# Kernel tuning notes

Measured on AMD Instinct MI355X. Metric: run time of the kernel, lower is better.

Reference implementation:

```python
import jax, jax.numpy as jnp
import numpy as np

N = 100          # num_objects
H = 128          # decoder_hidden
D = 128          # input_size (== H, required by the module's GRU linears)
REL = 7          # num_relative_features (use_3d=False)
E = N * (N - 1)  # fully-connected, no self loops
B = 32

_mask = ~np.eye(N, dtype=bool)
_SEND_NP, _RECV_NP = np.where(_mask)  # torch.where(~eye): rows=send, cols=recv
SEND = jnp.asarray(_SEND_NP, dtype=jnp.int32)
RECV = jnp.asarray(_RECV_NP, dtype=jnp.int32)


def setup_inputs() -> dict:
    key = jax.random.key(0)
    ks = jax.random.split(key, 34)
    def w(k, shape, scale=0.05):
        return jax.random.normal(k, shape, dtype=jnp.float32) * scale
    inp = {
        "inputs": jax.random.normal(ks[0], (B, N, D), jnp.float32),
        "edge_attr": jax.random.normal(ks[1], (B, E, REL + D), jnp.float32),
        "hidden": jax.random.normal(ks[2], (B, N, H), jnp.float32),
        # msg_mlp: Linear(2H,H) Tanh Linear(H,H) Tanh
        "msg_w1": w(ks[3], (2 * H, H)), "msg_b1": w(ks[4], (H,)),
        "msg_w2": w(ks[5], (H, H)),     "msg_b2": w(ks[6], (H,)),
        # present_msg_mlp: Linear(REL+D,H) ReLU Linear(H,H) ReLU
        "pm_w1": w(ks[7], (REL + D, H)), "pm_b1": w(ks[8], (H,)),
        "pm_w2": w(ks[9], (H, H)),       "pm_b2": w(ks[10], (H,)),
        # res_mlp: Linear(D,H) ReLU Linear(H,H) ReLU
        "res_w1": w(ks[11], (D, H)), "res_b1": w(ks[12], (H,)),
        "res_w2": w(ks[13], (H, H)), "res_b2": w(ks[14], (H,)),
        # GRU-style gates
        "ir_w": w(ks[15], (H, H)), "ir_b": w(ks[16], (H,)),
        "ii_w": w(ks[17], (H, H)), "ii_b": w(ks[18], (H,)),
        "in_w": w(ks[19], (H, H)), "in_b": w(ks[20], (H,)),
        "hr_w": w(ks[21], (H, H)),
        "hi_w": w(ks[22], (H, H)),
        "hh_w": w(ks[23], (H, H)),
        # out_mlp: Linear(H,H) ReLU Linear(H,H) ReLU Linear(H,D)
        "out_w1": w(ks[24], (H, H)), "out_b1": w(ks[25], (H,)),
        "out_w2": w(ks[26], (H, H)), "out_b2": w(ks[27], (H,)),
        "out_w3": w(ks[28], (H, D)), "out_b3": w(ks[29], (D,)),
    }
    return inp


def _scatter_mean(msgs, recv, num_nodes):
    # msgs: [B, E, H] -> [B, N, H], mean over incoming edges per node
    counts = jnp.zeros((num_nodes,), msgs.dtype).at[recv].add(1.0)
    summed = jnp.zeros((msgs.shape[0], num_nodes, msgs.shape[-1]), msgs.dtype)
    summed = summed.at[:, recv].add(msgs)
    return summed / counts[None, :, None]


def reference(inputs, edge_attr, hidden,
              msg_w1, msg_b1, msg_w2, msg_b2,
              pm_w1, pm_b1, pm_w2, pm_b2,
              res_w1, res_b1, res_w2, res_b2,
              ir_w, ir_b, ii_w, ii_b, in_w, in_b,
              hr_w, hi_w, hh_w,
              out_w1, out_b1, out_w2, out_b2, out_w3, out_b3):
    # gather hidden states along edges (dropout is identity: p=0 / eval)
    hm = jnp.concatenate([hidden[:, RECV], hidden[:, SEND]], axis=-1)  # [B,E,2H]
    hm = jnp.tanh(jnp.tanh(hm @ msg_w1 + msg_b1) @ msg_w2 + msg_b2)
    hidden_node = _scatter_mean(hm, RECV, N)                           # [B,N,H]

    pm = jax.nn.relu(jax.nn.relu(edge_attr @ pm_w1 + pm_b1) @ pm_w2 + pm_b2)
    present_node = _scatter_mean(pm, RECV, N)
    present_node = present_node + jax.nn.relu(
        jax.nn.relu(inputs @ res_w1 + res_b1) @ res_w2 + res_b2)

    r = jax.nn.sigmoid(present_node @ ir_w + ir_b + hidden_node @ hr_w)
    i = jax.nn.sigmoid(present_node @ ii_w + ii_b + hidden_node @ hi_w)
    n = jnp.tanh(present_node @ in_w + in_b + r * (hidden_node @ hh_w))
    hidden_new = (1.0 - i) * n + i * hidden

    pred = jax.nn.relu(hidden_new @ out_w1 + out_b1)
    pred = jax.nn.relu(pred @ out_w2 + out_b2)
    pred = pred @ out_w3 + out_b3
    return pred, hidden_new
```

## Files before the change

### kernel.cpp

```cpp
#include <hip/hip_runtime.h>

typedef unsigned short u16;
typedef unsigned int   u32;
typedef __attribute__((ext_vector_type(8))) short bf8;
typedef __attribute__((ext_vector_type(4))) float f4;

#define DF __device__ __forceinline__

DF float bf2f(u16 h){ u32 u = ((u32)h) << 16; float f; __builtin_memcpy(&f, &u, 4); return f; }
DF u16 f2bf(float f){ u32 u; __builtin_memcpy(&u, &f, 4); u = (u + 0x7FFFu + ((u >> 16) & 1u)) >> 16; return (u16)u; }
DF float fexp2(float x){ return __builtin_amdgcn_exp2f(x); }
DF float frcp (float x){ return __builtin_amdgcn_rcpf(x); }
DF float tanhF(float x){ float e = fexp2(2.8853900817779268f * x); return 1.0f - 2.0f * frcp(e + 1.0f); }
DF float sigF (float x){ return frcp(1.0f + fexp2(-1.4426950408889634f * x)); }
DF float4 ld4u(const float* p){ float4 v; __builtin_memcpy(&v, p, 16); return v; }
DF u32 cvtpk(float lo, float hi){ u32 r; asm("v_cvt_pk_bf16_f32 %0, %1, %2" : "=v"(r) : "v"(lo), "v"(hi)); return r; }

DF const bf8* fragp(const u16* packed, int w, int nt, int ks, int lane){
  return reinterpret_cast<const bf8*>(packed + (((w * 32 + nt * 4 + ks) * 64 + lane) * 8));
}
DF const bf8* fragp_pm1(const u16* packed, int nt, int ks, int lane){
  return reinterpret_cast<const bf8*>(packed + (((512 + nt * 5 + ks) * 64 + lane) * 8));
}

struct WPtrs { const float* p[16]; };

__global__ __launch_bounds__(256) void k_pack(WPtrs wp, u16* __restrict__ packed){
  int bi = blockIdx.x;
  int lane = threadIdx.x & 63, warp = threadIdx.x >> 6;
  if(bi == 16){
    const float* __restrict__ src = wp.p[14];
    u16* __restrict__ dst = packed + 512 * 64 * 8;
    for(int i = warp; i < 40; i += 4){
      int nt = i / 5, ks = i - nt * 5;
      int col = nt * 16 + (lane & 15);
      int kb  = ks * 32 + (lane >> 4) * 8;
      u16* o = dst + (i * 64 + lane) * 8;
      for(int j = 0; j < 8; j++){
        int row = kb + j;
        o[j] = (row < 135) ? f2bf(src[row * 128 + col]) : (u16)0;
      }
    }
    return;
  }
  const float* __restrict__ src = wp.p[bi];
  u16* __restrict__ dst = packed + bi * 32 * 64 * 8;
  for(int i = warp; i < 32; i += 4){
    int nt = i >> 2, ks = i & 3;
    int col = nt * 16 + (lane & 15);
    int kb  = ks * 32 + (lane >> 4) * 8;
    u16* o = dst + (i * 64 + lane) * 8;
    for(int j = 0; j < 8; j++) o[j] = f2bf(src[(kb + j) * 128 + col]);
  }
}

__global__ __launch_bounds__(512) void k_node_pre(
    const float* __restrict__ hidden, const float* __restrict__ inputs,
    const u16* __restrict__ packed,
    const float* __restrict__ res_b1, const float* __restrict__ res_b2,
    float* __restrict__ Ptop, float* __restrict__ Pbot, float* __restrict__ res2)
{
  __shared__ __align__(16) u16 hid[64 * 136];
  __shared__ __align__(16) u16 inp[64 * 136];
  __shared__ __align__(16) u16 t1s[64 * 136];
  int row0 = blockIdx.x * 64;
  int t = threadIdx.x, lane = t & 63, w = t >> 6;
  int lrow = lane & 15, lk = lane >> 4;
  for(int i = t; i < 64 * 128; i += 512){
    int rr = i >> 7, cc = i & 127;
    hid[rr * 136 + cc] = f2bf(hidden[(row0 + rr) * 128 + cc]);
    inp[rr * 136 + cc] = f2bf(inputs[(row0 + rr) * 128 + cc]);
  }
  bf8 f0[4], f1[4], f5[4], f6[4];
  #pragma unroll
  for(int k = 0; k < 4; k++){
    f0[k] = *fragp(packed, 0, w, k, lane);
    f1[k] = *fragp(packed, 1, w, k, lane);
    f5[k] = *fragp(packed, 5, w, k, lane);
    f6[k] = *fragp(packed, 6, w, k, lane);
  }
  int col = w * 16 + lrow;
  float rb1 = res_b1[col], rb2 = res_b2[col];
  __syncthreads();
  #pragma unroll
  for(int m = 0; m < 4; m++){
    bf8 a[4], a2[4];
    #pragma unroll
    for(int k = 0; k < 4; k++){
      a[k]  = *reinterpret_cast<const bf8*>(&hid[(m * 16 + lrow) * 136 + k * 32 + lk * 8]);
      a2[k] = *reinterpret_cast<const bf8*>(&inp[(m * 16 + lrow) * 136 + k * 32 + lk * 8]);
    }
    f4 c0 = {0.f,0.f,0.f,0.f}, c1 = {0.f,0.f,0.f,0.f}, c2 = {0.f,0.f,0.f,0.f};
    #pragma unroll
    for(int k = 0; k < 4; k++){
      c0 = __builtin_amdgcn_mfma_f32_16x16x32_bf16(a[k],  f0[k], c0, 0, 0, 0);
      c1 = __builtin_amdgcn_mfma_f32_16x16x32_bf16(a[k],  f1[k], c1, 0, 0, 0);
      c2 = __builtin_amdgcn_mfma_f32_16x16x32_bf16(a2[k], f5[k], c2, 0, 0, 0);
    }
    #pragma unroll
    for(int q = 0; q < 4; q++){
      int gr = row0 + m * 16 + lk * 4 + q;
      Ptop[gr * 128 + col] = c0[q];
      Pbot[gr * 128 + col] = c1[q];
      float v = c2[q] + rb1; v = v > 0.f ? v : 0.f;
      t1s[(m * 16 + lk * 4 + q) * 136 + col] = f2bf(v);
    }
  }
  __syncthreads();
  #pragma unroll
  for(int m = 0; m < 4; m++){
    bf8 a3[4];
    #pragma unroll
    for(int k = 0; k < 4; k++)
      a3[k] = *reinterpret_cast<const bf8*>(&t1s[(m * 16 + lrow) * 136 + k * 32 + lk * 8]);
    f4 c = {0.f,0.f,0.f,0.f};
    #pragma unroll
    for(int k = 0; k < 4; k++)
      c = __builtin_amdgcn_mfma_f32_16x16x32_bf16(a3[k], f6[k], c, 0, 0, 0);
    #pragma unroll
    for(int q = 0; q < 4; q++){
      float v = c[q] + rb2; v = v > 0.f ? v : 0.f;
      res2[(row0 + m * 16 + lk * 4 + q) * 128 + col] = v;
    }
  }
}

__global__ __launch_bounds__(256, 5) void k_edge(
    const float* __restrict__ EA,
    const float* __restrict__ Ptop, const float* __restrict__ Pbot,
    const float* __restrict__ msg_b1, const float* __restrict__ msg_b2,
    const float* __restrict__ pm_b1, const float* __restrict__ pm_b2,
    const u16* __restrict__ packed,
    float* __restrict__ hnode, float* __restrict__ pnode)
{
  __shared__ __align__(16) u16 bufA[112 * 128];
  __shared__ __align__(16) u16 tail[112 * 8];
  char* bb = (char*)bufA;
  char* tb = (char*)tail;
  int blk = blockIdx.x;
  int b = blk / 100, r = blk - b * 100;
  int t = threadIdx.x, lane = t & 63, w = t >> 6;
  int lrow = lane & 15, lk = lane >> 4;
  int n0 = 2 * w, n1 = 2 * w + 1;

  {
    bf8 w1a[5], w1b[5];
    #pragma unroll
    for(int k = 0; k < 5; k++){ w1a[k] = *fragp_pm1(packed, n0, k, lane); w1b[k] = *fragp_pm1(packed, n1, k, lane); }
    float b1a = pm_b1[n0 * 16 + lrow], b1b = pm_b1[n1 * 16 + lrow];
    for(int i = t; i < 99 * 16; i += 256){
      int row = i >> 4, g = i & 15;
      int s = row + (row >= r ? 1 : 0);
      int e = s * 99 + (r < s ? r : r - 1);
      const float* rp = EA + ((size_t)(b * 9900 + e)) * 135 + g * 8;
      float4 v0 = ld4u(rp), v1 = ld4u(rp + 4);
      u32 pk[4] = {cvtpk(v0.x, v0.y), cvtpk(v0.z, v0.w), cvtpk(v1.x, v1.y), cvtpk(v1.z, v1.w)};
      *reinterpret_cast<uint4*>(bb + row * 256 + ((g ^ (row & 7)) << 4)) = *reinterpret_cast<const uint4*>(pk);
    }
    for(int row = t; row < 99; row += 256){
      int s = row + (row >= r ? 1 : 0);
      int e = s * 99 + (r < s ? r : r - 1);
      const float* rp = EA + ((size_t)(b * 9900 + e)) * 135 + 128;
      float4 v0 = ld4u(rp);
      u32 pk[4] = {cvtpk(v0.x, v0.y), cvtpk(v0.z, v0.w), cvtpk(rp[4], rp[5]), cvtpk(rp[6], 0.f)};
      *reinterpret_cast<uint4*>(tb + row * 16) = *reinterpret_cast<const uint4*>(pk);
    }
    __syncthreads();
    #pragma unroll
    for(int m = 0; m < 7; m++){
      int arow = m * 16 + lrow;
      int sw = (arow & 7);
      bf8 a[5];
      #pragma unroll
      for(int k = 0; k < 4; k++)
        a[k] = *reinterpret_cast<const bf8*>(bb + arow * 256 + (((k * 4 + lk) ^ sw) << 4));
      bf8 a4 = {0,0,0,0,0,0,0,0};
      if(lk == 0) a4 = *reinterpret_cast<const bf8*>(tb + arow * 16);
      f4 c0 = {0.f,0.f,0.f,0.f}, c1 = {0.f,0.f,0.f,0.f};
      #pragma unroll
      for(int k = 0; k < 4; k++){
        c0 = __builtin_amdgcn_mfma_f32_16x16x32_bf16(a[k], w1a[k], c0, 0, 0, 0);
        c1 = __builtin_amdgcn_mfma_f32_16x16x32_bf16(a[k], w1b[k], c1, 0, 0, 0);
      }
      c0 = __builtin_amdgcn_mfma_f32_16x16x32_bf16(a4, w1a[4], c0, 0, 0, 0);
      c1 = __builtin_amdgcn_mfma_f32_16x16x32_bf16(a4, w1b[4], c1, 0, 0, 0);
      __syncthreads();
      #pragma unroll
      for(int qp = 0; qp < 2; qp++){
        float v0 = c0[2*qp]   + b1a; v0 = v0 > 0.f ? v0 : 0.f;
        float u0 = c0[2*qp+1] + b1a; u0 = u0 > 0.f ? u0 : 0.f;
        float v1 = c1[2*qp]   + b1b; v1 = v1 > 0.f ? v1 : 0.f;
        float u1 = c1[2*qp+1] + b1b; u1 = u1 > 0.f ? u1 : 0.f;
        u32 p0 = cvtpk(v0, u0), p1 = cvtpk(v1, u1);
        int row0_ = m * 16 + lk * 4 + 2 * qp;
        int sw0 = (row0_ & 7) << 4, sw1 = ((row0_ + 1) & 7) << 4;
        *reinterpret_cast<u16*>(bb + row0_ * 256       + (((n0 * 16 + lrow) * 2) ^ sw0)) = (u16)p0;
        *reinterpret_cast<u16*>(bb + (row0_ + 1) * 256 + (((n0 * 16 + lrow) * 2) ^ sw1)) = (u16)(p0 >> 16);
        *reinterpret_cast<u16*>(bb + row0_ * 256       + (((n1 * 16 + lrow) * 2) ^ sw0)) = (u16)p1;
        *reinterpret_cast<u16*>(bb + (row0_ + 1) * 256 + (((n1 * 16 + lrow) * 2) ^ sw1)) = (u16)(p1 >> 16);
      }
    }
    __syncthreads();
    bf8 w2a[4], w2b[4];
    #pragma unroll
    for(int k = 0; k < 4; k++){ w2a[k] = *fragp(packed, 15, n0, k, lane); w2b[k] = *fragp(packed, 15, n1, k, lane); }
    float b2a = pm_b2[n0 * 16 + lrow], b2b = pm_b2[n1 * 16 + lrow];
    float acc0 = 0.f, acc1 = 0.f;
    #pragma unroll
    for(int m = 0; m < 7; m++){
      int arow = m * 16 + lrow;
      int sw = (arow & 7);
      bf8 a[4];
      #pragma unroll
      for(int k = 0; k < 4; k++)
        a[k] = *reinterpret_cast<const bf8*>(bb + arow * 256 + (((k * 4 + lk) ^ sw) << 4));
      f4 c0 = {0.f,0.f,0.f,0.f}, c1 = {0.f,0.f,0.f,0.f};
      #pragma unroll
      for(int k = 0; k < 4; k++){
        c0 = __builtin_amdgcn_mfma_f32_16x16x32_bf16(a[k], w2a[k], c0, 0, 0, 0);
        c1 = __builtin_amdgcn_mfma_f32_16x16x32_bf16(a[k], w2b[k], c1, 0, 0, 0);
      }
      #pragma unroll
      for(int q = 0; q < 4; q++){
        int rr = m * 16 + lk * 4 + q;
        if(rr < 99){
          float v0 = c0[q] + b2a; acc0 += (v0 > 0.f ? v0 : 0.f);
          float v1 = c1[q] + b2b; acc1 += (v1 > 0.f ? v1 : 0.f);
        }
      }
    }
    acc0 += __shfl_xor(acc0, 16); acc0 += __shfl_xor(acc0, 32);
    acc1 += __shfl_xor(acc1, 16); acc1 += __shfl_xor(acc1, 32);
    if(lane < 16){
      float* dst = pnode + ((size_t)b * 100 + r) * 128;
      dst[n0 * 16 + lane] = acc0 * (1.0f / 99.0f);
      dst[n1 * 16 + lane] = acc1 * (1.0f / 99.0f);
    }
  }
  __syncthreads();

  {
    bf8 w2a[4], w2b[4];
    #pragma unroll
    for(int k = 0; k < 4; k++){ w2a[k] = *fragp(packed, 13, n0, k, lane); w2b[k] = *fragp(packed, 13, n1, k, lane); }
    float b2a = msg_b2[n0 * 16 + lrow], b2b = msg_b2[n1 * 16 + lrow];
    int c4 = t & 31;
    float4 pt = *reinterpret_cast<const float4*>(Ptop + ((size_t)b * 100 + r) * 128 + c4 * 4);
    float4 mb = *reinterpret_cast<const float4*>(msg_b1 + c4 * 4);
    pt.x += mb.x; pt.y += mb.y; pt.z += mb.z; pt.w += mb.w;
    for(int row = t >> 5; row < 99; row += 8){
      int s = row + (row >= r ? 1 : 0);
      float4 v = *reinterpret_cast<const float4*>(Pbot + ((size_t)b * 100 + s) * 128 + c4 * 4);
      u32 pk[2] = {cvtpk(tanhF(pt.x + v.x), tanhF(pt.y + v.y)),
                   cvtpk(tanhF(pt.z + v.z), tanhF(pt.w + v.w))};
      *reinterpret_cast<uint2*>(bb + row * 256 + ((8 * c4) ^ ((row & 7) << 4))) = *reinterpret_cast<const uint2*>(pk);
    }
    __syncthreads();
    float acc0 = 0.f, acc1 = 0.f;
    #pragma unroll
    for(int m = 0; m < 7; m++){
      int arow = m * 16 + lrow;
      int sw = (arow & 7);
      bf8 a[4];
      #pragma unroll
      for(int k = 0; k < 4; k++)
        a[k] = *reinterpret_cast<const bf8*>(bb + arow * 256 + (((k * 4 + lk) ^ sw) << 4));
      f4 c0 = {0.f,0.f,0.f,0.f}, c1 = {0.f,0.f,0.f,0.f};
      #pragma unroll
      for(int k = 0; k < 4; k++){
        c0 = __builtin_amdgcn_mfma_f32_16x16x32_bf16(a[k], w2a[k], c0, 0, 0, 0);
        c1 = __builtin_amdgcn_mfma_f32_16x16x32_bf16(a[k], w2b[k], c1, 0, 0, 0);
      }
      #pragma unroll
      for(int q = 0; q < 4; q++){
        int rr = m * 16 + lk * 4 + q;
        if(rr < 99){
          acc0 += tanhF(c0[q] + b2a);
          acc1 += tanhF(c1[q] + b2b);
        }
      }
    }
    acc0 += __shfl_xor(acc0, 16); acc0 += __shfl_xor(acc0, 32);
    acc1 += __shfl_xor(acc1, 16); acc1 += __shfl_xor(acc1, 32);
    if(lane < 16){
      float* dst = hnode + ((size_t)b * 100 + r) * 128;
      dst[n0 * 16 + lane] = acc0 * (1.0f / 99.0f);
      dst[n1 * 16 + lane] = acc1 * (1.0f / 99.0f);
    }
  }
}

__global__ __launch_bounds__(512) void k_final(
    const float* __restrict__ hnode, const float* __restrict__ pnode,
    const float* __restrict__ res2, const float* __restrict__ hidden,
    const u16* __restrict__ packed,
    const float* __restrict__ ir_b, const float* __restrict__ ii_b, const float* __restrict__ in_b,
    const float* __restrict__ ob1, const float* __restrict__ ob2, const float* __restrict__ ob3,
    float* __restrict__ out_pred, float* __restrict__ out_hid)
{
  __shared__ __align__(16) u16 hn[64 * 136];
  __shared__ __align__(16) u16 pr[64 * 136];
  __shared__ __align__(16) u16 hw[64 * 136];
  int row0 = blockIdx.x * 64;
  int t = threadIdx.x, lane = t & 63, w = t >> 6;
  int lrow = lane & 15, lk = lane >> 4;
  for(int i = t; i < 64 * 128; i += 512){
    int rr = i >> 7, cc = i & 127;
    hn[rr * 136 + cc] = f2bf(hnode[(row0 + rr) * 128 + cc]);
    pr[rr * 136 + cc] = f2bf(pnode[(row0 + rr) * 128 + cc] + res2[(row0 + rr) * 128 + cc]);
  }
  int col = w * 16 + lrow;
  bf8 mhr[4], mhi[4], mhh[4], mir[4], mii[4], min_[4];
  #pragma unroll
  for(int k = 0; k < 4; k++){
    mhr[k]  = *fragp(packed, 2, w, k, lane);
    mhi[k]  = *fragp(packed, 3, w, k, lane);
    mhh[k]  = *fragp(packed, 4, w, k, lane);
    mir[k]  = *fragp(packed, 7, w, k, lane);
    mii[k]  = *fragp(packed, 8, w, k, lane);
    min_[k] = *fragp(packed, 9, w, k, lane);
  }
  float bir = ir_b[col], bii = ii_b[col], bin = in_b[col];
  __syncthreads();
  #pragma unroll
  for(int m = 0; m < 4; m++){
    bf8 a[4], p[4];
    #pragma unroll
    for(int k = 0; k < 4; k++){
      a[k] = *reinterpret_cast<const bf8*>(&hn[(m * 16 + lrow) * 136 + k * 32 + lk * 8]);
      p[k] = *reinterpret_cast<const bf8*>(&pr[(m * 16 + lrow) * 136 + k * 32 + lk * 8]);
    }
    f4 cR = {0.f,0.f,0.f,0.f}, cI = {0.f,0.f,0.f,0.f}, cN = {0.f,0.f,0.f,0.f};
    f4 dR = {0.f,0.f,0.f,0.f}, dI = {0.f,0.f,0.f,0.f}, dN = {0.f,0.f,0.f,0.f};
    #pragma unroll
    for(int k = 0; k < 4; k++){
      cR = __builtin_amdgcn_mfma_f32_16x16x32_bf16(a[k], mhr[k],  cR, 0, 0, 0);
      cI = __builtin_amdgcn_mfma_f32_16x16x32_bf16(a[k], mhi[k],  cI, 0, 0, 0);
      cN = __builtin_amdgcn_mfma_f32_16x16x32_bf16(a[k], mhh[k],  cN, 0, 0, 0);
      dR = __builtin_amdgcn_mfma_f32_16x16x32_bf16(p[k], mir[k],  dR, 0, 0, 0);
      dI = __builtin_amdgcn_mfma_f32_16x16x32_bf16(p[k], mii[k],  dI, 0, 0, 0);
      dN = __builtin_amdgcn_mfma_f32_16x16x32_bf16(p[k], min_[k], dN, 0, 0, 0);
    }
    #pragma unroll
    for(int q = 0; q < 4; q++){
      int gr = row0 + m * 16 + lk * 4 + q;
      float rv = sigF(dR[q] + bir + cR[q]);
      float iv = sigF(dI[q] + bii + cI[q]);
      float nv = tanhF(dN[q] + bin + rv * cN[q]);
      float hold = hidden[gr * 128 + col];
      float hnew = (1.f - iv) * nv + iv * hold;
      out_hid[gr * 128 + col] = hnew;
      hw[(m * 16 + lk * 4 + q) * 136 + col] = f2bf(hnew);
    }
  }
  __syncthreads();
  {
    bf8 m10[4];
    #pragma unroll
    for(int k = 0; k < 4; k++) m10[k] = *fragp(packed, 10, w, k, lane);
    float bb = ob1[col];
    #pragma unroll
    for(int m = 0; m < 4; m++){
      f4 c = {0.f,0.f,0.f,0.f};
      #pragma unroll
      for(int k = 0; k < 4; k++){
        bf8 a = *reinterpret_cast<const bf8*>(&hw[(m * 16 + lrow) * 136 + k * 32 + lk * 8]);
        c = __builtin_amdgcn_mfma_f32_16x16x32_bf16(a, m10[k], c, 0, 0, 0);
      }
      #pragma unroll
      for(int q = 0; q < 4; q++){
        float v = c[q] + bb; v = v > 0.f ? v : 0.f;
        hn[(m * 16 + lk * 4 + q) * 136 + col] = f2bf(v);
      }
    }
  }
  __syncthreads();
  {
    bf8 m11[4];
    #pragma unroll
    for(int k = 0; k < 4; k++) m11[k] = *fragp(packed, 11, w, k, lane);
    float bb = ob2[col];
    #pragma unroll
    for(int m = 0; m < 4; m++){
      f4 c = {0.f,0.f,0.f,0.f};
      #pragma unroll
      for(int k = 0; k < 4; k++){
        bf8 a = *reinterpret_cast<const bf8*>(&hn[(m * 16 + lrow) * 136 + k * 32 + lk * 8]);
        c = __builtin_amdgcn_mfma_f32_16x16x32_bf16(a, m11[k], c, 0, 0, 0);
      }
      #pragma unroll
      for(int q = 0; q < 4; q++){
        float v = c[q] + bb; v = v > 0.f ? v : 0.f;
        pr[(m * 16 + lk * 4 + q) * 136 + col] = f2bf(v);
      }
    }
  }
  __syncthreads();
  {
    bf8 m12[4];
    #pragma unroll
    for(int k = 0; k < 4; k++) m12[k] = *fragp(packed, 12, w, k, lane);
    float bb = ob3[col];
    #pragma unroll
    for(int m = 0; m < 4; m++){
      f4 c = {0.f,0.f,0.f,0.f};
      #pragma unroll
      for(int k = 0; k < 4; k++){
        bf8 a = *reinterpret_cast<const bf8*>(&pr[(m * 16 + lrow) * 136 + k * 32 + lk * 8]);
        c = __builtin_amdgcn_mfma_f32_16x16x32_bf16(a, m12[k], c, 0, 0, 0);
      }
      #pragma unroll
      for(int q = 0; q < 4; q++)
        out_pred[(row0 + m * 16 + lk * 4 + q) * 128 + col] = c[q] + bb;
    }
  }
}

extern "C" void kernel_launch(void* const* d_in, const int* in_sizes, int n_in,
                              void* d_out, int out_size, void* d_ws, size_t ws_size,
                              hipStream_t stream)
{
  const float* inputs = (const float*)d_in[0];
  const float* edge   = (const float*)d_in[1];
  const float* hidden = (const float*)d_in[2];
  const float* msg_w1 = (const float*)d_in[3];
  const float* msg_b1 = (const float*)d_in[4];
  const float* msg_w2 = (const float*)d_in[5];
  const float* msg_b2 = (const float*)d_in[6];
  const float* pm_w1  = (const float*)d_in[7];
  const float* pm_b1  = (const float*)d_in[8];
  const float* pm_w2  = (const float*)d_in[9];
  const float* pm_b2  = (const float*)d_in[10];
  const float* res_w1 = (const float*)d_in[11];
  const float* res_b1 = (const float*)d_in[12];
  const float* res_w2 = (const float*)d_in[13];
  const float* res_b2 = (const float*)d_in[14];
  const float* ir_w = (const float*)d_in[15]; const float* ir_b = (const float*)d_in[16];
  const float* ii_w = (const float*)d_in[17]; const float* ii_b = (const float*)d_in[18];
  const float* in_w = (const float*)d_in[19]; const float* in_b = (const float*)d_in[20];
  const float* hr_w = (const float*)d_in[21];
  const float* hi_w = (const float*)d_in[22];
  const float* hh_w = (const float*)d_in[23];
  const float* out_w1 = (const float*)d_in[24]; const float* out_b1 = (const float*)d_in[25];
  const float* out_w2 = (const float*)d_in[26]; const float* out_b2 = (const float*)d_in[27];
  const float* out_w3 = (const float*)d_in[28]; const float* out_b3 = (const float*)d_in[29];

  char* ws = (char*)d_ws;
  u16*   packed = (u16*)ws;
  float* Ptop   = (float*)(ws + (1 << 20));
  float* Pbot   = (float*)(ws + (1 << 20) + 1 * 1638400);
  float* res2   = (float*)(ws + (1 << 20) + 2 * 1638400);
  float* hnode  = (float*)(ws + (1 << 20) + 3 * 1638400);
  float* pnode  = (float*)(ws + (1 << 20) + 4 * 1638400);

  WPtrs wp;
  wp.p[0]  = msg_w1;
  wp.p[1]  = msg_w1 + 128 * 128;
  wp.p[2]  = hr_w;  wp.p[3]  = hi_w;  wp.p[4]  = hh_w;
  wp.p[5]  = res_w1; wp.p[6] = res_w2;
  wp.p[7]  = ir_w;  wp.p[8]  = ii_w;  wp.p[9]  = in_w;
  wp.p[10] = out_w1; wp.p[11] = out_w2; wp.p[12] = out_w3;
  wp.p[13] = msg_w2; wp.p[14] = pm_w1; wp.p[15] = pm_w2;

  k_pack<<<17, 256, 0, stream>>>(wp, packed);
  k_node_pre<<<50, 512, 0, stream>>>(hidden, inputs, packed, res_b1, res_b2, Ptop, Pbot, res2);
  k_edge<<<3200, 256, 0, stream>>>(edge, Ptop, Pbot, msg_b1, msg_b2, pm_b1, pm_b2,
                                   packed, hnode, pnode);
  float* outp = (float*)d_out;
  k_final<<<50, 512, 0, stream>>>(hnode, pnode, res2, hidden, packed,
                                  ir_b, ii_b, in_b, out_b1, out_b2, out_b3,
                                  outp, outp + 32 * 100 * 128);
}
```

Baseline: 141.3 us.

## Batch pm layer-1 MFMA tiles to cut in-place barriers from seven to two

The first present-message layer wrote its ReLU output back into the same shared buffer, so every 16-row tile needed a block-wide barrier before its store. Now the first four tiles are computed and held in registers, followed by one barrier and their stores, then the last three tiles go through the same pattern. The weight-fragment loads also move after the edge-attribute staging loop, and the occupancy hint drops from 5 to 4 blocks per CU to make room for the extra live accumulators. The aim is to remove barrier stalls at the cost of more registers and possibly lower occupancy.

Result: faster. 118.7 us (-16.0%).

```diff
diff --git a/kernel.cpp b/kernel.cpp
--- a/kernel.cpp
+++ b/kernel.cpp
@@ -125,7 +125,7 @@
   }
 }
 
-__global__ __launch_bounds__(256, 5) void k_edge(
+__global__ __launch_bounds__(256, 4) void k_edge(
     const float* __restrict__ EA,
     const float* __restrict__ Ptop, const float* __restrict__ Pbot,
     const float* __restrict__ msg_b1, const float* __restrict__ msg_b2,
@@ -144,10 +144,6 @@
   int n0 = 2 * w, n1 = 2 * w + 1;
 
   {
-    bf8 w1a[5], w1b[5];
-    #pragma unroll
-    for(int k = 0; k < 5; k++){ w1a[k] = *fragp_pm1(packed, n0, k, lane); w1b[k] = *fragp_pm1(packed, n1, k, lane); }
-    float b1a = pm_b1[n0 * 16 + lrow], b1b = pm_b1[n1 * 16 + lrow];
     for(int i = t; i < 99 * 16; i += 256){
       int row = i >> 4, g = i & 15;
       int s = row + (row >= r ? 1 : 0);
@@ -165,12 +161,17 @@
       u32 pk[4] = {cvtpk(v0.x, v0.y), cvtpk(v0.z, v0.w), cvtpk(rp[4], rp[5]), cvtpk(rp[6], 0.f)};
       *reinterpret_cast<uint4*>(tb + row * 16) = *reinterpret_cast<const uint4*>(pk);
     }
+    bf8 w1a[5], w1b[5];
+    #pragma unroll
+    for(int k = 0; k < 5; k++){ w1a[k] = *fragp_pm1(packed, n0, k, lane); w1b[k] = *fragp_pm1(packed, n1, k, lane); }
+    float b1a = pm_b1[n0 * 16 + lrow], b1b = pm_b1[n1 * 16 + lrow];
     __syncthreads();
-    #pragma unroll
-    for(int m = 0; m < 7; m++){
-      int arow = m * 16 + lrow;
-      int sw = (arow & 7);
-      bf8 a[5];
+
+    f4 cA0[4], cA1[4];
+    #pragma unroll
+    for(int m = 0; m < 4; m++){
+      int arow = m * 16 + lrow, sw = arow & 7;
+      bf8 a[4];
       #pragma unroll
       for(int k = 0; k < 4; k++)
         a[k] = *reinterpret_cast<const bf8*>(bb + arow * 256 + (((k * 4 + lk) ^ sw) << 4));
@@ -184,13 +185,18 @@
       }
       c0 = __builtin_amdgcn_mfma_f32_16x16x32_bf16(a4, w1a[4], c0, 0, 0, 0);
       c1 = __builtin_amdgcn_mfma_f32_16x16x32_bf16(a4, w1b[4], c1, 0, 0, 0);
-      __syncthreads();
+      cA0[m] = c0; cA1[m] = c1;
+    }
+    __syncthreads();
+
+    #pragma unroll
+    for(int m = 0; m < 4; m++){
       #pragma unroll
       for(int qp = 0; qp < 2; qp++){
-        float v0 = c0[2*qp]   + b1a; v0 = v0 > 0.f ? v0 : 0.f;
-        float u0 = c0[2*qp+1] + b1a; u0 = u0 > 0.f ? u0 : 0.f;
-        float v1 = c1[2*qp]   + b1b; v1 = v1 > 0.f ? v1 : 0.f;
-        float u1 = c1[2*qp+1] + b1b; u1 = u1 > 0.f ? u1 : 0.f;
+        float v0 = cA0[m][2*qp]   + b1a; v0 = v0 > 0.f ? v0 : 0.f;
+        float u0 = cA0[m][2*qp+1] + b1a; u0 = u0 > 0.f ? u0 : 0.f;
+        float v1 = cA1[m][2*qp]   + b1b; v1 = v1 > 0.f ? v1 : 0.f;
+        float u1 = cA1[m][2*qp+1] + b1b; u1 = u1 > 0.f ? u1 : 0.f;
         u32 p0 = cvtpk(v0, u0), p1 = cvtpk(v1, u1);
         int row0_ = m * 16 + lk * 4 + 2 * qp;
         int sw0 = (row0_ & 7) << 4, sw1 = ((row0_ + 1) & 7) << 4;
@@ -200,7 +206,47 @@
         *reinterpret_cast<u16*>(bb + (row0_ + 1) * 256 + (((n1 * 16 + lrow) * 2) ^ sw1)) = (u16)(p1 >> 16);
       }
     }
+    f4 cB0[3], cB1[3];
+    #pragma unroll
+    for(int m = 0; m < 3; m++){
+      int arow = (m + 4) * 16 + lrow, sw = arow & 7;
+      bf8 a[4];
+      #pragma unroll
+      for(int k = 0; k < 4; k++)
+        a[k] = *reinterpret_cast<const bf8*>(bb + arow * 256 + (((k * 4 + lk) ^ sw) << 4));
+      bf8 a4 = {0,0,0,0,0,0,0,0};
+      if(lk == 0) a4 = *reinterpret_cast<const bf8*>(tb + arow * 16);
+      f4 c0 = {0.f,0.f,0.f,0.f}, c1 = {0.f,0.f,0.f,0.f};
+      #pragma unroll
+      for(int k = 0; k < 4; k++){
+        c0 = __builtin_amdgcn_mfma_f32_16x16x32_bf16(a[k], w1a[k], c0, 0, 0, 0);
+        c1 = __builtin_amdgcn_mfma_f32_16x16x32_bf16(a[k], w1b[k], c1, 0, 0, 0);
+      }
+      c0 = __builtin_amdgcn_mfma_f32_16x16x32_bf16(a4, w1a[4], c0, 0, 0, 0);
+      c1 = __builtin_amdgcn_mfma_f32_16x16x32_bf16(a4, w1b[4], c1, 0, 0, 0);
+      cB0[m] = c0; cB1[m] = c1;
+    }
     __syncthreads();
+
+    #pragma unroll
+    for(int m = 0; m < 3; m++){
+      #pragma unroll
+      for(int qp = 0; qp < 2; qp++){
+        float v0 = cB0[m][2*qp]   + b1a; v0 = v0 > 0.f ? v0 : 0.f;
+        float u0 = cB0[m][2*qp+1] + b1a; u0 = u0 > 0.f ? u0 : 0.f;
+        float v1 = cB1[m][2*qp]   + b1b; v1 = v1 > 0.f ? v1 : 0.f;
+        float u1 = cB1[m][2*qp+1] + b1b; u1 = u1 > 0.f ? u1 : 0.f;
+        u32 p0 = cvtpk(v0, u0), p1 = cvtpk(v1, u1);
+        int row0_ = (m + 4) * 16 + lk * 4 + 2 * qp;
+        int sw0 = (row0_ & 7) << 4, sw1 = ((row0_ + 1) & 7) << 4;
+        *reinterpret_cast<u16*>(bb + row0_ * 256       + (((n0 * 16 + lrow) * 2) ^ sw0)) = (u16)p0;
+        *reinterpret_cast<u16*>(bb + (row0_ + 1) * 256 + (((n0 * 16 + lrow) * 2) ^ sw1)) = (u16)(p0 >> 16);
+        *reinterpret_cast<u16*>(bb + row0_ * 256       + (((n1 * 16 + lrow) * 2) ^ sw0)) = (u16)p1;
+        *reinterpret_cast<u16*>(bb + (row0_ + 1) * 256 + (((n1 * 16 + lrow) * 2) ^ sw1)) = (u16)(p1 >> 16);
+      }
+    }
+    __syncthreads();
+
     bf8 w2a[4], w2b[4];
     #pragma unroll
     for(int k = 0; k < 4; k++){ w2a[k] = *fragp(packed, 15, n0, k, lane); w2b[k] = *fragp(packed, 15, n1, k, lane); }
@@ -208,8 +254,7 @@
     float acc0 = 0.f, acc1 = 0.f;
     #pragma unroll
     for(int m = 0; m < 7; m++){
-      int arow = m * 16 + lrow;
-      int sw = (arow & 7);
+      int arow = m * 16 + lrow, sw = arow & 7;
       bf8 a[4];
       #pragma unroll
       for(int k = 0; k < 4; k++)
@@ -259,8 +304,7 @@
     float acc0 = 0.f, acc1 = 0.f;
     #pragma unroll
     for(int m = 0; m < 7; m++){
-      int arow = m * 16 + lrow;
-      int sw = (arow & 7);
+      int arow = m * 16 + lrow, sw = arow & 7;
       bf8 a[4];
       #pragma unroll
       for(int k = 0; k < 4; k++)
```
